# Kernel tuning notes

Hardware: AMD Instinct MI355X
Metric: run time of the kernel (lower is better)

Reference implementation:

```python
import jax, jax.numpy as jnp
import numpy as np

DIM = 768
HEADS = 12
HEAD_DIM = DIM // HEADS
SCALE = HEAD_DIM ** -0.5


def setup_inputs() -> dict:
    key = jax.random.key(0)
    k1, k2, k3, k4, k5 = jax.random.split(key, 5)
    B, N = 4, 2048
    x = jax.random.normal(k1, (B, N, DIM), dtype=jnp.float32)
    # qkv Linear: weight [3*dim, dim], bias [3*dim]
    w_qkv = jax.random.normal(k2, (3 * DIM, DIM), dtype=jnp.float32) * (DIM ** -0.5)
    b_qkv = jax.random.normal(k3, (3 * DIM,), dtype=jnp.float32) * 0.01
    # proj Linear: weight [dim, dim], bias [dim]
    w_proj = jax.random.normal(k4, (DIM, DIM), dtype=jnp.float32) * (DIM ** -0.5)
    b_proj = jax.random.normal(k5, (DIM,), dtype=jnp.float32) * 0.01
    return {"x": x, "w_qkv": w_qkv, "b_qkv": b_qkv, "w_proj": w_proj, "b_proj": b_proj}


def reference(x, w_qkv, b_qkv, w_proj, b_proj):
    B, N, C = x.shape
    qkv = (jnp.einsum('bnc,oc->bno', x, w_qkv) + b_qkv)
    qkv = qkv.reshape(B, N, 3, HEADS, HEAD_DIM).transpose(2, 0, 3, 1, 4)
    q, k, v = qkv[0], qkv[1], qkv[2]
    attn = jnp.einsum('bhqd,bhkd->bhqk', q, k) * SCALE
    attn = jax.nn.softmax(attn, axis=-1)
    out = jnp.einsum('bhqk,bhkd->bhqd', attn, v)  # [B, H, N, Dh]
    out = out.transpose(0, 2, 1, 3).reshape(B, N, C)
    # dropout is identity in eval mode
    return jnp.einsum('bnc,oc->bno', out, w_proj) + b_proj
```

## Files before the change

### kernel.cpp

```cpp
#include <hip/hip_runtime.h>
#include <hip/hip_bf16.h>

using bf16 = __hip_bfloat16;
typedef __bf16 bf16x8 __attribute__((ext_vector_type(8)));
typedef short short4v __attribute__((ext_vector_type(4)));
typedef short short8v __attribute__((ext_vector_type(8)));
typedef float float4v __attribute__((ext_vector_type(4)));

#define DIM   768
#define NH    12
#define HD    64
#define SEQ   2048
#define BATCH 4
#define TOK   (BATCH * SEQ)
#define SCALE_QL2E 0.18033688011112042f

#define NX  (TOK * DIM)
#define NWQ (3 * DIM * DIM)
#define NWP (DIM * DIM)

__device__ __forceinline__ short f2bf(float f) {
  union { bf16 h; short s; } u;
  u.h = __float2bfloat16(f);
  return u.s;
}

union frag8 { short4v h[2]; short8v s; bf16x8 b; };

__device__ __forceinline__ void async_copy16(const bf16* g, short* l) {
  __builtin_amdgcn_global_load_lds(
      (const __attribute__((address_space(1))) unsigned int*)g,
      (__attribute__((address_space(3))) unsigned int*)l, 16, 0, 0);
}

__global__ void __launch_bounds__(256)
cvt3(const float* __restrict__ a, bf16* __restrict__ oa, long na,
     const float* __restrict__ b, bf16* __restrict__ ob, long nb,
     const float* __restrict__ c, bf16* __restrict__ oc, long nc) {
  const long i = ((long)blockIdx.x * 256 + threadIdx.x) * 8;
  const float* src; bf16* dst; long off;
  if (i < na)                { src = a; dst = oa; off = i; }
  else if (i < na + nb)      { src = b; dst = ob; off = i - na; }
  else if (i < na + nb + nc) { src = c; dst = oc; off = i - na - nb; }
  else return;
  const float4v x0 = *(const float4v*)(src + off);
  const float4v x1 = *(const float4v*)(src + off + 4);
  short8v r;
  r[0] = f2bf(x0[0]); r[1] = f2bf(x0[1]); r[2] = f2bf(x0[2]); r[3] = f2bf(x0[3]);
  r[4] = f2bf(x1[0]); r[5] = f2bf(x1[1]); r[6] = f2bf(x1[2]); r[7] = f2bf(x1[3]);
  *(short8v*)(dst + off) = r;
}

__device__ __forceinline__ void gemm_mainloop(const bf16* __restrict__ A,
                                              const bf16* __restrict__ B,
                                              short* As, short* Bs,
                                              float4v acc[4][4]) {
  const int t = threadIdx.x;
  const int w = t >> 6, l = t & 63, lr = l & 15, q = l >> 4;
  const int wr = ((w >> 1) << 6), wc = ((w & 1) << 6);

  const bf16* Ag = A + (t >> 2) * DIM + (t & 3) * 8;
  const bf16* Bg = B + (t >> 2) * DIM + (t & 3) * 8;

  for (int k0 = 0; k0 < DIM; k0 += 32) {
    __syncthreads();
    async_copy16(Ag,            &As[t * 8]);
    async_copy16(Ag + 64 * DIM, &As[2048 + t * 8]);
    async_copy16(Bg,            &Bs[t * 8]);
    async_copy16(Bg + 64 * DIM, &Bs[2048 + t * 8]);
    Ag += 32; Bg += 32;
    __syncthreads();

    bf16x8 af[4], bfv[4];
#pragma unroll
    for (int i = 0; i < 4; ++i)
      af[i] = *(const bf16x8*)&As[(wr + i * 16 + lr) * 32 + q * 8];
#pragma unroll
    for (int j = 0; j < 4; ++j)
      bfv[j] = *(const bf16x8*)&Bs[(wc + j * 16 + lr) * 32 + q * 8];
#pragma unroll
    for (int i = 0; i < 4; ++i)
#pragma unroll
      for (int j = 0; j < 4; ++j)
        acc[i][j] = __builtin_amdgcn_mfma_f32_16x16x32_bf16(af[i], bfv[j],
                                                            acc[i][j], 0, 0, 0);
  }
}

#define STG(gp, c, slot, k0)                                                  \
  async_copy16((gp) + (k0),      &lds[c][slot][t * 8]);                       \
  async_copy16((gp) + (k0) + 32, &lds[c][slot][4096 + t * 8])

#define RD_A(dst, C, slot)                                                    \
  _Pragma("unroll") for (int f_ = 0; f_ < 4; ++f_) {                          \
    dst[f_][0] = *(const bf16x8*)&lds[C][slot][f_ * 1024 + arow32 + acol];    \
    dst[f_][1] = *(const bf16x8*)&lds[C][slot][4096 + f_ * 1024 + arow32 + acol]; \
  }

#define RD_B(dst, C, slot)                                                    \
  _Pragma("unroll") for (int g_ = 0; g_ < 2; ++g_) {                          \
    dst[g_][0] = *(const bf16x8*)&lds[C][slot][g_ * 2048 + brow32 + acol];    \
    dst[g_][1] = *(const bf16x8*)&lds[C][slot][4096 + g_ * 2048 + brow32 + acol]; \
  }

#define MFMA8(AF, BF, MO, NO)                                                 \
  _Pragma("unroll") for (int f_ = 0; f_ < 4; ++f_)                            \
  _Pragma("unroll") for (int g_ = 0; g_ < 2; ++g_) {                          \
    acc[(MO) + f_][(NO) + g_] = __builtin_amdgcn_mfma_f32_16x16x32_bf16(      \
        AF[f_][0], BF[g_][0], acc[(MO) + f_][(NO) + g_], 0, 0, 0);            \
    acc[(MO) + f_][(NO) + g_] = __builtin_amdgcn_mfma_f32_16x16x32_bf16(      \
        AF[f_][1], BF[g_][1], acc[(MO) + f_][(NO) + g_], 0, 0, 0);            \
  }

#define BARRIER __builtin_amdgcn_s_barrier()
#define LGKM0 asm volatile("s_waitcnt lgkmcnt(0)" ::: "memory")
#define VW6 asm volatile("s_waitcnt vmcnt(6)" ::: "memory")
#define VW0 asm volatile("s_waitcnt vmcnt(0)" ::: "memory")
#define NOSTG (void)0

#define KTILE(C, ST1, ST2, ST3, ST4, VW)                                      \
  {                                                                           \
    bf16x8 a0[4][2], a1[4][2], b0[2][2], b1[2][2];                            \
    RD_A(a0, C, 0); RD_B(b0, C, 2);                                           \
    ST1; BARRIER; LGKM0;                                                      \
    __builtin_amdgcn_s_setprio(1); MFMA8(a0, b0, 0, 0);                       \
    __builtin_amdgcn_s_setprio(0); BARRIER;                                   \
    RD_B(b1, C, 3);                                                           \
    ST2; BARRIER; LGKM0;                                                      \
    __builtin_amdgcn_s_setprio(1); MFMA8(a0, b1, 0, 2);                       \
    __builtin_amdgcn_s_setprio(0); BARRIER;                                   \
    RD_A(a1, C, 1);                                                           \
    ST3; BARRIER; LGKM0;                                                      \
    __builtin_amdgcn_s_setprio(1); MFMA8(a1, b0, 4, 0);                       \
    __builtin_amdgcn_s_setprio(0); BARRIER;                                   \
    ST4; BARRIER;                                                             \
    __builtin_amdgcn_s_setprio(1); MFMA8(a1, b1, 4, 2);                       \
    __builtin_amdgcn_s_setprio(0); VW; BARRIER;                               \
  }

__global__ void __launch_bounds__(512, 2)
gemm_qkv(const bf16* __restrict__ X, const bf16* __restrict__ W,
         const float* __restrict__ bias,
         bf16* __restrict__ qb, bf16* __restrict__ kb, bf16* __restrict__ vb) {
  __shared__ short lds[2][4][8192];
  const int t = threadIdx.x;
  const int w = t >> 6, l = t & 63, lr = l & 15, q = l >> 4;
  const int wm = w >> 2, wn = w & 3;

  const int orig = blockIdx.x;
  const int swz = (orig & 7) * 36 + (orig >> 3);
  const int tm = swz / 9, tn = swz - tm * 9;
  const int row0 = tm * 256, col0 = tn * 256;

  const int sr = t >> 2;
  const int scol = (((t & 3) << 3) ^ (((sr >> 1) & 3) << 3));
  const bf16* pa0 = X + (size_t)(row0 +       sr) * DIM + scol;
  const bf16* pa1 = X + (size_t)(row0 + 128 + sr) * DIM + scol;
  const bf16* pb0 = W + (size_t)(col0 +       sr) * DIM + scol;
  const bf16* pb1 = W + (size_t)(col0 + 128 + sr) * DIM + scol;

  const int acol = ((q << 3) ^ (((lr >> 1) & 3) << 3));
  const int arow32 = (wm * 16 + lr) * 32;
  const int brow32 = (wn * 16 + lr) * 32;

  float4v acc[8][4] = {};

  STG(pa0, 0, 0, 0);
  STG(pb0, 0, 2, 0);
  STG(pb1, 0, 3, 0);
  STG(pa1, 0, 1, 0);
  STG(pa0, 1, 0, 64);
  STG(pb0, 1, 2, 64);
  STG(pb1, 1, 3, 64);
  asm volatile("s_waitcnt vmcnt(6)" ::: "memory");
  BARRIER;

#pragma unroll 1
  for (int i = 0; i < 5; ++i) {
    KTILE(0, STG(pa1, 1, 1, 64),  STG(pa0, 0, 0, 128),
             STG(pb0, 0, 2, 128), STG(pb1, 0, 3, 128), VW6);
    KTILE(1, STG(pa1, 0, 1, 128), STG(pa0, 1, 0, 192),
             STG(pb0, 1, 2, 192), STG(pb1, 1, 3, 192), VW6);
    pa0 += 128; pa1 += 128; pb0 += 128; pb1 += 128;
  }
  KTILE(0, STG(pa1, 1, 1, 64), NOSTG, NOSTG, NOSTG, VW0);
  KTILE(1, NOSTG, NOSTG, NOSTG, NOSTG, NOSTG);

#pragma unroll
  for (int nf = 0; nf < 4; ++nf) {
    const int gn = col0 + nf * 64 + wn * 16 + lr;
    const int which = gn / DIM;
    const int cc = gn - which * DIM;
    const int hh = cc >> 6, dd = cc & 63;
    const float bv = bias[gn];
#pragma unroll
    for (int mf = 0; mf < 8; ++mf) {
      const int gm0 = row0 + mf * 32 + wm * 16 + (q << 2);
      const int b = gm0 >> 11, n0 = gm0 & 2047;
      if (which == 2) {
        short4v pv;
#pragma unroll
        for (int r = 0; r < 4; ++r) pv[r] = f2bf(acc[mf][nf][r] + bv);
        *(short4v*)&vb[((size_t)(b * NH + hh) * HD + dd) * SEQ + n0] = pv;
      } else {
        bf16* dst = (which == 0) ? qb : kb;
        const float sc = (which == 0) ? SCALE_QL2E : 1.0f;
#pragma unroll
        for (int r = 0; r < 4; ++r)
          dst[((size_t)(b * NH + hh) * SEQ + n0 + r) * HD + dd] =
              __float2bfloat16((acc[mf][nf][r] + bv) * sc);
      }
    }
  }
}

__global__ void __launch_bounds__(256, 3)
flash_attn(const bf16* __restrict__ Qp, const bf16* __restrict__ Kp,
           const bf16* __restrict__ Vtp, bf16* __restrict__ Op) {
  const int bh = blockIdx.y, qt = blockIdx.x;
  const int t = threadIdx.x, w = t >> 6, l = t & 63, lr = l & 15, q = l >> 4;
  __shared__ short Ks[2][64 * 68];
  __shared__ short Vt[2][64 * 66];

  const bf16* Qb = Qp  + (size_t)(bh * SEQ + qt * 128) * HD;
  const bf16* Kb = Kp  + (size_t)bh * SEQ * HD;
  const bf16* Vb = Vtp + (size_t)bh * HD * SEQ;

  const int tr3 = t >> 3, td8 = (t & 7) * 8;

#pragma unroll
  for (int i = 0; i < 4; ++i) {
    const int row = i * 32 + tr3;
    *(short8v*)&Ks[row >> 6][(row & 63) * 68 + td8] =
        *(const short8v*)(Qb + (size_t)row * HD + td8);
  }
  __syncthreads();
  bf16x8 qf[2][2];
#pragma unroll
  for (int it = 0; it < 2; ++it)
#pragma unroll
    for (int kq = 0; kq < 2; ++kq) {
      const int row = w * 32 + it * 16 + lr;
      qf[it][kq] = *(const bf16x8*)&Ks[row >> 6][(row & 63) * 68 + kq * 32 + q * 8];
    }
  __syncthreads();

  short8v kr[2], vr[2];
#pragma unroll
  for (int i = 0; i < 2; ++i) {
    kr[i] = *(const short8v*)(Kb + (size_t)(i * 32 + tr3) * HD + td8);
    vr[i] = *(const short8v*)(Vb + (size_t)(i * 32 + tr3) * SEQ + td8);
  }

  frag8 ones;
#pragma unroll
  for (int r = 0; r < 8; ++r) ones.s[r] = (short)0x3F80;

  float4v o[2][4] = {};
  float4v lacc[2] = {};

  for (int kt = 0; kt < 32; ++kt) {
    const int cur = kt & 1;
#pragma unroll
    for (int i = 0; i < 2; ++i) {
      *(short8v*)&Ks[cur][(i * 32 + tr3) * 68 + td8] = kr[i];
      *(short8v*)&Vt[cur][(i * 32 + tr3) * 66 + td8] = vr[i];
    }
    if (kt < 31) {
      const int k1 = (kt + 1) * 64;
#pragma unroll
      for (int i = 0; i < 2; ++i) {
        kr[i] = *(const short8v*)(Kb + (size_t)(k1 + i * 32 + tr3) * HD + td8);
        vr[i] = *(const short8v*)(Vb + (size_t)(i * 32 + tr3) * SEQ + k1 + td8);
      }
    }
    __syncthreads();

    float4v s[4][2] = {};
    __builtin_amdgcn_s_setprio(1);
#pragma unroll
    for (int jn = 0; jn < 4; ++jn) {
      bf16x8 kf[2];
#pragma unroll
      for (int kq = 0; kq < 2; ++kq)
        kf[kq] = *(const bf16x8*)&Ks[cur][(jn * 16 + lr) * 68 + kq * 32 + q * 8];
#pragma unroll
      for (int it = 0; it < 2; ++it)
#pragma unroll
        for (int kq = 0; kq < 2; ++kq)
          s[jn][it] = __builtin_amdgcn_mfma_f32_16x16x32_bf16(kf[kq], qf[it][kq],
                                                              s[jn][it], 0, 0, 0);
    }
    __builtin_amdgcn_s_setprio(0);

    frag8 pf[2][2];
#pragma unroll
    for (int it = 0; it < 2; ++it)
#pragma unroll
      for (int c4 = 0; c4 < 2; ++c4)
#pragma unroll
        for (int r = 0; r < 4; ++r) {
          pf[c4][it].s[r]     = f2bf(__builtin_amdgcn_exp2f(s[2 * c4][it][r]));
          pf[c4][it].s[4 + r] = f2bf(__builtin_amdgcn_exp2f(s[2 * c4 + 1][it][r]));
        }

    __builtin_amdgcn_s_setprio(1);
#pragma unroll
    for (int c4 = 0; c4 < 2; ++c4) {
#pragma unroll
      for (int dj = 0; dj < 4; ++dj) {
        frag8 vf;
        vf.h[0] = *(const short4v*)&Vt[cur][(dj * 16 + lr) * 66 + c4 * 32 + (q << 2)];
        vf.h[1] = *(const short4v*)&Vt[cur][(dj * 16 + lr) * 66 + c4 * 32 + 16 + (q << 2)];
#pragma unroll
        for (int it = 0; it < 2; ++it)
          o[it][dj] = __builtin_amdgcn_mfma_f32_16x16x32_bf16(pf[c4][it].b, vf.b,
                                                              o[it][dj], 0, 0, 0);
      }
#pragma unroll
      for (int it = 0; it < 2; ++it)
        lacc[it] = __builtin_amdgcn_mfma_f32_16x16x32_bf16(pf[c4][it].b, ones.b,
                                                           lacc[it], 0, 0, 0);
    }
    __builtin_amdgcn_s_setprio(0);
  }

  const int b = bh / NH, h = bh - b * NH;
#pragma unroll
  for (int it = 0; it < 2; ++it)
#pragma unroll
    for (int r = 0; r < 4; ++r) {
      const float linv = 1.0f / lacc[it][r];
      const int grow = b * SEQ + qt * 128 + w * 32 + it * 16 + (q << 2) + r;
      bf16* orow = Op + (size_t)grow * DIM + h * HD;
#pragma unroll
      for (int dj = 0; dj < 4; ++dj)
        orow[dj * 16 + lr] = __float2bfloat16(o[it][dj][r] * linv);
    }
}

__global__ void __launch_bounds__(256)
gemm_proj(const bf16* __restrict__ A, const bf16* __restrict__ W,
          const float* __restrict__ bias, float* __restrict__ out) {
  __shared__ short As[128 * 32];
  __shared__ short Bs[128 * 32];
  const int t = threadIdx.x;
  const int w = t >> 6, l = t & 63, lr = l & 15, q = l >> 4;
  const int wr = ((w >> 1) << 6), wc = ((w & 1) << 6);
  const int row0 = blockIdx.y * 128, col0 = blockIdx.x * 128;

  float4v acc[4][4] = {};
  gemm_mainloop(A + row0 * DIM, W + col0 * DIM, As, Bs, acc);

#pragma unroll
  for (int j = 0; j < 4; ++j) {
    const int gn = col0 + wc + j * 16 + lr;
    const float bv = bias[gn];
#pragma unroll
    for (int i = 0; i < 4; ++i) {
#pragma unroll
      for (int r = 0; r < 4; ++r) {
        const int gm = row0 + wr + i * 16 + (q << 2) + r;
        out[(size_t)gm * DIM + gn] = acc[i][j][r] + bv;
      }
    }
  }
}

extern "C" void kernel_launch(void* const* d_in, const int* in_sizes, int n_in,
                              void* d_out, int out_size, void* d_ws, size_t ws_size,
                              hipStream_t stream) {
  const float* x      = (const float*)d_in[0];
  const float* w_qkv  = (const float*)d_in[1];
  const float* b_qkv  = (const float*)d_in[2];
  const float* w_proj = (const float*)d_in[3];
  const float* b_proj = (const float*)d_in[4];
  float* out = (float*)d_out;

  const size_t perbuf = (size_t)BATCH * NH * SEQ * HD;
  bf16* qb  = (bf16*)d_ws;
  bf16* kb  = qb + perbuf;
  bf16* vb  = kb + perbuf;
  bf16* ao  = vb + perbuf;
  bf16* xb  = ao + perbuf;
  bf16* wqb = xb + (size_t)NX;
  bf16* wpb = wqb + (size_t)NWQ;

  const int cvt_blocks = (NX + NWQ + NWP) / 8 / 256;
  cvt3<<<cvt_blocks, 256, 0, stream>>>(x, xb, NX, w_qkv, wqb, NWQ, w_proj, wpb, NWP);
  gemm_qkv <<<dim3(288), 512, 0, stream>>>(xb, wqb, b_qkv, qb, kb, vb);
  flash_attn<<<dim3(SEQ / 128, BATCH * NH), 256, 0, stream>>>(qb, kb, vb, ao);
  gemm_proj <<<dim3(DIM / 128, TOK / 128),  256, 0, stream>>>(ao, wpb, b_proj, out);
}
```

Baseline: 218.1 us.

## Retile QKV GEMM to 256x288 blocks with triple-buffered K=32 pipeline

The QKV projection GEMM now uses 256x288 output tiles, so the grid has 256 blocks instead of 288. That count matches the 256 CUs and avoids a partial second wave. The k-loop changes from a double-buffered K=64 scheme with four sub-phases to a fully unrolled triple-buffered K=32 pipeline with one barrier pair per phase. The extra 32 rows of B are loaded with 4-byte async copies. Each warp now holds a 4x9 fragment tile, which raises register pressure and may change LDS bank behaviour.

```diff
diff --git a/kernel.cpp b/kernel.cpp
--- a/kernel.cpp
+++ b/kernel.cpp
@@ -31,6 +31,11 @@
   __builtin_amdgcn_global_load_lds(
       (const __attribute__((address_space(1))) unsigned int*)g,
       (__attribute__((address_space(3))) unsigned int*)l, 16, 0, 0);
+}
+__device__ __forceinline__ void async_copy4(const bf16* g, short* l) {
+  __builtin_amdgcn_global_load_lds(
+      (const __attribute__((address_space(1))) unsigned int*)g,
+      (__attribute__((address_space(3))) unsigned int*)l, 4, 0, 0);
 }
 
 __global__ void __launch_bounds__(256)
@@ -87,115 +92,102 @@
   }
 }
 
-#define STG(gp, c, slot, k0)                                                  \
-  async_copy16((gp) + (k0),      &lds[c][slot][t * 8]);                       \
-  async_copy16((gp) + (k0) + 32, &lds[c][slot][4096 + t * 8])
-
-#define RD_A(dst, C, slot)                                                    \
-  _Pragma("unroll") for (int f_ = 0; f_ < 4; ++f_) {                          \
-    dst[f_][0] = *(const bf16x8*)&lds[C][slot][f_ * 1024 + arow32 + acol];    \
-    dst[f_][1] = *(const bf16x8*)&lds[C][slot][4096 + f_ * 1024 + arow32 + acol]; \
-  }
-
-#define RD_B(dst, C, slot)                                                    \
-  _Pragma("unroll") for (int g_ = 0; g_ < 2; ++g_) {                          \
-    dst[g_][0] = *(const bf16x8*)&lds[C][slot][g_ * 2048 + brow32 + acol];    \
-    dst[g_][1] = *(const bf16x8*)&lds[C][slot][4096 + g_ * 2048 + brow32 + acol]; \
-  }
-
-#define MFMA8(AF, BF, MO, NO)                                                 \
-  _Pragma("unroll") for (int f_ = 0; f_ < 4; ++f_)                            \
-  _Pragma("unroll") for (int g_ = 0; g_ < 2; ++g_) {                          \
-    acc[(MO) + f_][(NO) + g_] = __builtin_amdgcn_mfma_f32_16x16x32_bf16(      \
-        AF[f_][0], BF[g_][0], acc[(MO) + f_][(NO) + g_], 0, 0, 0);            \
-    acc[(MO) + f_][(NO) + g_] = __builtin_amdgcn_mfma_f32_16x16x32_bf16(      \
-        AF[f_][1], BF[g_][1], acc[(MO) + f_][(NO) + g_], 0, 0, 0);            \
-  }
-
+#define VW5 asm volatile("s_waitcnt vmcnt(5)" ::: "memory")
+#define VW0 asm volatile("s_waitcnt vmcnt(0)" ::: "memory")
 #define BARRIER __builtin_amdgcn_s_barrier()
 #define LGKM0 asm volatile("s_waitcnt lgkmcnt(0)" ::: "memory")
-#define VW6 asm volatile("s_waitcnt vmcnt(6)" ::: "memory")
-#define VW0 asm volatile("s_waitcnt vmcnt(0)" ::: "memory")
 #define NOSTG (void)0
-
-#define KTILE(C, ST1, ST2, ST3, ST4, VW)                                      \
-  {                                                                           \
-    bf16x8 a0[4][2], a1[4][2], b0[2][2], b1[2][2];                            \
-    RD_A(a0, C, 0); RD_B(b0, C, 2);                                           \
-    ST1; BARRIER; LGKM0;                                                      \
-    __builtin_amdgcn_s_setprio(1); MFMA8(a0, b0, 0, 0);                       \
-    __builtin_amdgcn_s_setprio(0); BARRIER;                                   \
-    RD_B(b1, C, 3);                                                           \
-    ST2; BARRIER; LGKM0;                                                      \
-    __builtin_amdgcn_s_setprio(1); MFMA8(a0, b1, 0, 2);                       \
-    __builtin_amdgcn_s_setprio(0); BARRIER;                                   \
-    RD_A(a1, C, 1);                                                           \
-    ST3; BARRIER; LGKM0;                                                      \
-    __builtin_amdgcn_s_setprio(1); MFMA8(a1, b0, 4, 0);                       \
-    __builtin_amdgcn_s_setprio(0); BARRIER;                                   \
-    ST4; BARRIER;                                                             \
-    __builtin_amdgcn_s_setprio(1); MFMA8(a1, b1, 4, 2);                       \
-    __builtin_amdgcn_s_setprio(0); VW; BARRIER;                               \
-  }
+#define NOVW  (void)0
+
+#define STGP(s, p)                                                            \
+  async_copy16(pa + (p) * 32,             &As[s][t * 8]);                     \
+  async_copy16(pa + 128 * DIM + (p) * 32, &As[s][4096 + t * 8]);              \
+  async_copy16(pb + (p) * 32,             &Bs[s][t * 8]);                     \
+  async_copy16(pb + 128 * DIM + (p) * 32, &Bs[s][4096 + t * 8]);              \
+  async_copy4 (pb3 + (p) * 32,            &Bs[s][8192 + t * 2])
+
+#define PHASE(RS, STG_, VW_) {                                                \
+  bf16x8 af[4], bfv[9];                                                       \
+  _Pragma("unroll") for (int mf_ = 0; mf_ < 4; ++mf_)                         \
+    af[mf_] = *(const bf16x8*)&As[RS][mf_ * 512 + arow];                      \
+  _Pragma("unroll") for (int nf_ = 0; nf_ < 9; ++nf_)                         \
+    bfv[nf_] = *(const bf16x8*)&Bs[RS][nf_ * 512 + brow];                     \
+  STG_; BARRIER; LGKM0;                                                       \
+  __builtin_amdgcn_s_setprio(1);                                              \
+  _Pragma("unroll") for (int mf_ = 0; mf_ < 4; ++mf_)                         \
+  _Pragma("unroll") for (int nf_ = 0; nf_ < 9; ++nf_)                         \
+    acc[mf_][nf_] = __builtin_amdgcn_mfma_f32_16x16x32_bf16(                  \
+        af[mf_], bfv[nf_], acc[mf_][nf_], 0, 0, 0);                           \
+  __builtin_amdgcn_s_setprio(0); VW_; BARRIER; }
 
 __global__ void __launch_bounds__(512, 2)
 gemm_qkv(const bf16* __restrict__ X, const bf16* __restrict__ W,
          const float* __restrict__ bias,
          bf16* __restrict__ qb, bf16* __restrict__ kb, bf16* __restrict__ vb) {
-  __shared__ short lds[2][4][8192];
+  __shared__ short As[3][256 * 32];
+  __shared__ short Bs[3][288 * 32];
   const int t = threadIdx.x;
   const int w = t >> 6, l = t & 63, lr = l & 15, q = l >> 4;
-  const int wm = w >> 2, wn = w & 3;
+  const int wm = w >> 1, wn = w & 1;
 
   const int orig = blockIdx.x;
-  const int swz = (orig & 7) * 36 + (orig >> 3);
-  const int tm = swz / 9, tn = swz - tm * 9;
-  const int row0 = tm * 256, col0 = tn * 256;
+  const int swz = (orig & 7) * 32 + (orig >> 3);
+  const int tm = swz >> 3, tn = swz & 7;
+  const int row0 = tm * 256, col0 = tn * 288;
 
   const int sr = t >> 2;
   const int scol = (((t & 3) << 3) ^ (((sr >> 1) & 3) << 3));
-  const bf16* pa0 = X + (size_t)(row0 +       sr) * DIM + scol;
-  const bf16* pa1 = X + (size_t)(row0 + 128 + sr) * DIM + scol;
-  const bf16* pb0 = W + (size_t)(col0 +       sr) * DIM + scol;
-  const bf16* pb1 = W + (size_t)(col0 + 128 + sr) * DIM + scol;
+  const bf16* pa  = X + (size_t)(row0 + sr) * DIM + scol;
+  const bf16* pb  = W + (size_t)(col0 + sr) * DIM + scol;
+  const int r3 = 256 + (t >> 4);
+  const int c3 = ((t & 15) << 1) ^ (((r3 >> 1) & 3) << 3);
+  const bf16* pb3 = W + (size_t)(col0 + r3) * DIM + c3;
 
   const int acol = ((q << 3) ^ (((lr >> 1) & 3) << 3));
-  const int arow32 = (wm * 16 + lr) * 32;
-  const int brow32 = (wn * 16 + lr) * 32;
-
-  float4v acc[8][4] = {};
-
-  STG(pa0, 0, 0, 0);
-  STG(pb0, 0, 2, 0);
-  STG(pb1, 0, 3, 0);
-  STG(pa1, 0, 1, 0);
-  STG(pa0, 1, 0, 64);
-  STG(pb0, 1, 2, 64);
-  STG(pb1, 1, 3, 64);
-  asm volatile("s_waitcnt vmcnt(6)" ::: "memory");
-  BARRIER;
-
-#pragma unroll 1
-  for (int i = 0; i < 5; ++i) {
-    KTILE(0, STG(pa1, 1, 1, 64),  STG(pa0, 0, 0, 128),
-             STG(pb0, 0, 2, 128), STG(pb1, 0, 3, 128), VW6);
-    KTILE(1, STG(pa1, 0, 1, 128), STG(pa0, 1, 0, 192),
-             STG(pb0, 1, 2, 192), STG(pb1, 1, 3, 192), VW6);
-    pa0 += 128; pa1 += 128; pb0 += 128; pb1 += 128;
-  }
-  KTILE(0, STG(pa1, 1, 1, 64), NOSTG, NOSTG, NOSTG, VW0);
-  KTILE(1, NOSTG, NOSTG, NOSTG, NOSTG, NOSTG);
-
-#pragma unroll
-  for (int nf = 0; nf < 4; ++nf) {
-    const int gn = col0 + nf * 64 + wn * 16 + lr;
+  const int arow = (wm * 64 + lr) * 32 + acol;
+  const int brow = (wn * 144 + lr) * 32 + acol;
+
+  float4v acc[4][9] = {};
+
+  STGP(0, 0);
+  STGP(1, 1);
+  VW5; BARRIER;
+
+  PHASE(0, STGP(2, 2),  VW5)
+  PHASE(1, STGP(0, 3),  VW5)
+  PHASE(2, STGP(1, 4),  VW5)
+  PHASE(0, STGP(2, 5),  VW5)
+  PHASE(1, STGP(0, 6),  VW5)
+  PHASE(2, STGP(1, 7),  VW5)
+  PHASE(0, STGP(2, 8),  VW5)
+  PHASE(1, STGP(0, 9),  VW5)
+  PHASE(2, STGP(1, 10), VW5)
+  PHASE(0, STGP(2, 11), VW5)
+  PHASE(1, STGP(0, 12), VW5)
+  PHASE(2, STGP(1, 13), VW5)
+  PHASE(0, STGP(2, 14), VW5)
+  PHASE(1, STGP(0, 15), VW5)
+  PHASE(2, STGP(1, 16), VW5)
+  PHASE(0, STGP(2, 17), VW5)
+  PHASE(1, STGP(0, 18), VW5)
+  PHASE(2, STGP(1, 19), VW5)
+  PHASE(0, STGP(2, 20), VW5)
+  PHASE(1, STGP(0, 21), VW5)
+  PHASE(2, STGP(1, 22), VW5)
+  PHASE(0, STGP(2, 23), VW5)
+  PHASE(1, NOSTG,       VW0)
+  PHASE(2, NOSTG,       NOVW)
+
+#pragma unroll
+  for (int nf = 0; nf < 9; ++nf) {
+    const int gn = col0 + wn * 144 + nf * 16 + lr;
     const int which = gn / DIM;
     const int cc = gn - which * DIM;
     const int hh = cc >> 6, dd = cc & 63;
     const float bv = bias[gn];
 #pragma unroll
-    for (int mf = 0; mf < 8; ++mf) {
-      const int gm0 = row0 + mf * 32 + wm * 16 + (q << 2);
+    for (int mf = 0; mf < 4; ++mf) {
+      const int gm0 = row0 + wm * 64 + mf * 16 + (q << 2);
       const int b = gm0 >> 11, n0 = gm0 & 2047;
       if (which == 2) {
         short4v pv;
@@ -388,7 +380,7 @@
 
   const int cvt_blocks = (NX + NWQ + NWP) / 8 / 256;
   cvt3<<<cvt_blocks, 256, 0, stream>>>(x, xb, NX, w_qkv, wqb, NWQ, w_proj, wpb, NWP);
-  gemm_qkv <<<dim3(288), 512, 0, stream>>>(xb, wqb, b_qkv, qb, kb, vb);
+  gemm_qkv <<<dim3(256), 512, 0, stream>>>(xb, wqb, b_qkv, qb, kb, vb);
   flash_attn<<<dim3(SEQ / 128, BATCH * NH), 256, 0, stream>>>(qb, kb, vb, ao);
   gemm_proj <<<dim3(DIM / 128, TOK / 128),  256, 0, stream>>>(ao, wpb, b_proj, out);
 }
```

Result: faster. 207.8 us (-4.7%).
